# Kernel tuning notes

Measured on AMD Instinct MI355X. Metric: run time of the kernel, lower is better.

Reference implementation:

```python
import jax, jax.numpy as jnp
import numpy as np
import math

N, S, T, E, H = 2, 2048, 2048, 1024, 16
HD = E // H  # head_dim = 64


def setup_inputs() -> dict:
    key = jax.random.key(0)
    ks = jax.random.split(key, 11)
    scale = 1.0 / math.sqrt(E)
    inp = {
        "query": jax.random.normal(ks[0], (N, S, E), jnp.float32),
        "key": jax.random.normal(ks[1], (N, T, E), jnp.float32),
        "value": jax.random.normal(ks[2], (N, T, E), jnp.float32),
        "Wq": jax.random.normal(ks[3], (E, E), jnp.float32) * scale,
        "bq": jnp.zeros((E,), jnp.float32),
        "Wk": jax.random.normal(ks[4], (E, E), jnp.float32) * scale,
        "bk": jnp.zeros((E,), jnp.float32),
        "Wv": jax.random.normal(ks[5], (E, E), jnp.float32) * scale,
        "bv": jnp.zeros((E,), jnp.float32),
        "Wo": jax.random.normal(ks[6], (E, E), jnp.float32) * scale,
        "bo": jnp.zeros((E,), jnp.float32),
    }
    return inp


def reference(query, key, value, Wq, bq, Wk, bk, Wv, bv, Wo, bo):
    # QKV projections, then split heads: [N, S, E] -> [N, H, S, HD]
    q = (query @ Wq + bq).reshape(N, S, H, HD).transpose(0, 2, 1, 3)
    k = (key @ Wk + bk).reshape(N, T, H, HD).transpose(0, 2, 1, 3)
    v = (value @ Wv + bv).reshape(N, T, H, HD).transpose(0, 2, 1, 3)
    # scaled dot-product attention scores [N, H, S, T]
    scores = jnp.einsum('nhse,nhte->nhst', q, k) / math.sqrt(HD)
    attn = jax.nn.softmax(scores, axis=-1)
    # dropout is identity in eval mode
    out = jnp.einsum('nhst,nhte->nhse', attn, v)  # [N, H, S, HD]
    out = out.transpose(0, 2, 1, 3).reshape(N, S, E)
    return out @ Wo + bo
```

## Files before the change

kernel.cpp:

```cpp
#include <hip/hip_runtime.h>
#include <hip/hip_bf16.h>

typedef __bf16 bf16x8 __attribute__((ext_vector_type(8)));
typedef __bf16 bf16x4 __attribute__((ext_vector_type(4)));
typedef float  f32x4  __attribute__((ext_vector_type(4)));
typedef float  f32x16 __attribute__((ext_vector_type(16)));

#define MFMA16(a, b, c) __builtin_amdgcn_mfma_f32_16x16x32_bf16((a), (b), (c), 0, 0, 0)
#define MFMA32(a, b, c) __builtin_amdgcn_mfma_f32_32x32x16_bf16((a), (b), (c), 0, 0, 0)

constexpr int SEQ = 2048, EMB = 1024, NHEAD = 16, HD = 64;
constexpr float SSCALE = 0.18033688f;

__device__ __forceinline__ void glds16(const void* g, void* l) {
    __builtin_amdgcn_global_load_lds(
        (const __attribute__((address_space(1))) void*)g,
        (__attribute__((address_space(3))) void*)l, 16, 0, 0);
}

__global__ __launch_bounds__(256)
void prep(const float* __restrict__ W0, const float* __restrict__ W1,
          const float* __restrict__ W2, const float* __restrict__ W3,
          __bf16* __restrict__ T0, __bf16* __restrict__ T1,
          __bf16* __restrict__ T2, __bf16* __restrict__ T3,
          const float* __restrict__ X0, const float* __restrict__ X1,
          const float* __restrict__ X2, __bf16* __restrict__ Y0,
          __bf16* __restrict__ Y1, __bf16* __restrict__ Y2)
{
    __shared__ float tile[32][33];
    const int z = blockIdx.z;
    if (z < 4) {
        const float* W = (z==0) ? W0 : (z==1) ? W1 : (z==2) ? W2 : W3;
        __bf16*      T = (z==0) ? T0 : (z==1) ? T1 : (z==2) ? T2 : T3;
        const float s = (z == 0) ? SSCALE : 1.0f;
        const int kb = blockIdx.x * 32, nb = blockIdx.y * 32;
        const int c = threadIdx.x & 31, r0 = threadIdx.x >> 5;
#pragma unroll
        for (int i = 0; i < 4; ++i)
            tile[r0 + 8*i][c] = W[(size_t)(kb + r0 + 8*i)*1024 + nb + c];
        __syncthreads();
#pragma unroll
        for (int i = 0; i < 4; ++i)
            T[(size_t)(nb + r0 + 8*i)*1024 + kb + c] = (__bf16)(tile[c][r0 + 8*i] * s);
    } else {
        const float* X = (z==4) ? X0 : (z==5) ? X1 : X2;
        __bf16*      Y = (z==4) ? Y0 : (z==5) ? Y1 : Y2;
        const size_t base =
            ((size_t)(blockIdx.y * 32 + blockIdx.x) * 256 + threadIdx.x) * 16;
#pragma unroll
        for (int j = 0; j < 2; ++j) {
            const float4* s4 = (const float4*)(X + base + j*8);
            float4 f0 = s4[0], f1 = s4[1];
            bf16x8 v;
            v[0]=(__bf16)f0.x; v[1]=(__bf16)f0.y; v[2]=(__bf16)f0.z; v[3]=(__bf16)f0.w;
            v[4]=(__bf16)f1.x; v[5]=(__bf16)f1.y; v[6]=(__bf16)f1.z; v[7]=(__bf16)f1.w;
            *(bf16x8*)(Y + base + j*8) = v;
        }
    }
}

struct GArg { const __bf16* A; const __bf16* Bt; const float* bias; void* C;
              int mode; int kbase; int kcount; float bscale; };
struct GArgs3 { GArg a[3]; };

__global__ __launch_bounds__(256)
void gemmk(GArgs3 args)
{
    const GArg g = args.a[blockIdx.z];
    __shared__ __attribute__((aligned(16))) __bf16 As[128*64];
    __shared__ __attribute__((aligned(16))) __bf16 Bs[128*64];
    const int tid = threadIdx.x, lane = tid & 63, wave = tid >> 6;
    const int wm = wave >> 1, wn = wave & 1;
    const int quad = lane >> 4, l16 = lane & 15;
    const int bm = blockIdx.x, bn = blockIdx.y;

    f32x4 acc[4][4] = {};

    for (int kt = 0; kt < g.kcount; ++kt) {
        const int k0 = g.kbase + kt*64;
        __syncthreads();
#pragma unroll
        for (int j = 0; j < 4; ++j) {
            const int ci = j*256 + tid;
            const int row = ci >> 3, cg = ((ci & 7) ^ (row & 7)) * 8;
            glds16(g.A + (size_t)(bm*128 + row)*1024 + k0 + cg,
                   &As[(j*256 + wave*64)*8]);
        }
#pragma unroll
        for (int j = 0; j < 4; ++j) {
            const int ci = j*256 + tid;
            const int row = ci >> 3, cg = ((ci & 7) ^ (row & 7)) * 8;
            glds16(g.Bt + (size_t)(bn*128 + row)*1024 + k0 + cg,
                   &Bs[(j*256 + wave*64)*8]);
        }
        __syncthreads();
#pragma unroll
        for (int ks = 0; ks < 2; ++ks) {
            const int kc = ks*4 + quad;
            bf16x8 af[4], bfr[4];
#pragma unroll
            for (int mt = 0; mt < 4; ++mt) {
                const int ar = wm*64 + mt*16 + l16;
                af[mt] = *(const bf16x8*)&As[ar*64 + (kc ^ (ar & 7))*8];
            }
#pragma unroll
            for (int nt = 0; nt < 4; ++nt) {
                const int br = wn*64 + nt*16 + l16;
                bfr[nt] = *(const bf16x8*)&Bs[br*64 + (kc ^ (br & 7))*8];
            }
#pragma unroll
            for (int mt = 0; mt < 4; ++mt)
#pragma unroll
                for (int nt = 0; nt < 4; ++nt)
                    acc[mt][nt] = MFMA16(af[mt], bfr[nt], acc[mt][nt]);
        }
    }

#pragma unroll
    for (int nt = 0; nt < 4; ++nt) {
        const int n = bn*128 + wn*64 + nt*16 + l16;
        const float bvs = (g.bias ? g.bias[n] : 0.f) * g.bscale;
#pragma unroll
        for (int mt = 0; mt < 4; ++mt) {
            const int mbase = bm*128 + wm*64 + mt*16 + quad*4;
            f32x4 v = acc[mt][nt];
            if (g.mode == 0) {
                __bf16* C = (__bf16*)g.C;
                const int h = n >> 6, d = n & 63;
#pragma unroll
                for (int r = 0; r < 4; ++r) {
                    const int m = mbase + r;
                    const int nb = m >> 11, s = m & 2047;
                    C[(size_t)(nb*NHEAD + h)*(SEQ*HD) + (size_t)s*HD + d] = (__bf16)(v[r] + bvs);
                }
            } else if (g.mode == 1) {
                __bf16* C = (__bf16*)g.C;
                const int h = n >> 6, d = n & 63;
                const int nb = mbase >> 11, s = mbase & 2047;
                const int tg = (s >> 2) & 7;
                const int pg = (tg & 4) | ((tg & 1) << 1) | ((tg & 2) >> 1);
                const int sp = (s & ~31) | (pg << 2);
                bf16x4 o;
#pragma unroll
                for (int r = 0; r < 4; ++r) o[r] = (__bf16)(v[r] + bvs);
                *(bf16x4*)&C[(size_t)(nb*NHEAD + h)*(SEQ*HD) + (size_t)d*SEQ + sp] = o;
            } else {
                float* C = (float*)g.C;
#pragma unroll
                for (int r = 0; r < 4; ++r)
                    C[(size_t)(mbase + r)*1024 + n] = v[r] + bvs;
            }
        }
    }
}

__global__ __launch_bounds__(256)
void attn32(const __bf16* __restrict__ qg, const __bf16* __restrict__ kg,
            const __bf16* __restrict__ vg, __bf16* __restrict__ Og)
{
    __shared__ __attribute__((aligned(16))) __bf16 Ks[128*64];
    __shared__ __attribute__((aligned(16))) __bf16 Vs[64*128];

    const int tid = threadIdx.x, lane = tid & 63, wave = tid >> 6;
    const int l32 = lane & 31, half = lane >> 5;
    const int nh = blockIdx.y;
    const int q0 = blockIdx.x * 128;
    const __bf16* qb = qg + (size_t)nh * (SEQ*HD);
    const __bf16* kb = kg + (size_t)nh * (SEQ*HD);
    const __bf16* vb = vg + (size_t)nh * (SEQ*HD);

    bf16x8 qf[4];
#pragma unroll
    for (int ks = 0; ks < 4; ++ks)
        qf[ks] = *(const bf16x8*)(qb + (size_t)(q0 + wave*32 + l32)*HD + ks*16 + half*8);

    bf16x8 vone;
#pragma unroll
    for (int i = 0; i < 8; ++i) vone[i] = (__bf16)1.0f;

    f32x16 oacc[2] = {};
    f32x16 osum = {};

    for (int t0 = 0; t0 < SEQ; t0 += 128) {
        __syncthreads();
#pragma unroll
        for (int j = 0; j < 4; ++j) {
            const int ci = j*256 + tid;
            const int row = ci >> 3, cg = ((ci & 7) ^ (row & 7)) * 8;
            glds16(kb + (size_t)(t0 + row)*HD + cg, &Ks[(j*256 + wave*64)*8]);
        }
#pragma unroll
        for (int j = 0; j < 4; ++j) {
            const int ci = j*256 + tid;
            const int row = ci >> 4, cg = ((ci & 15) ^ (row & 7)) * 8;
            glds16(vb + (size_t)row*SEQ + t0 + cg, &Vs[(j*256 + wave*64)*8]);
        }
        __syncthreads();

        f32x16 sc[4] = {};
#pragma unroll
        for (int ks = 0; ks < 4; ++ks) {
            const int c = ks*2 + half;
#pragma unroll
            for (int nt = 0; nt < 4; ++nt) {
                const int kr = nt*32 + l32;
                bf16x8 kf = *(const bf16x8*)&Ks[kr*64 + ((c ^ (kr & 7))*8)];
                sc[nt] = MFMA32(kf, qf[ks], sc[nt]);
            }
        }

#pragma unroll
        for (int nt = 0; nt < 4; ++nt)
#pragma unroll
            for (int sub = 0; sub < 2; ++sub) {
                bf16x8 pf;
#pragma unroll
                for (int j = 0; j < 8; ++j)
                    pf[j] = (__bf16)exp2f(sc[nt][sub*8 + j]);
                const int c2 = (nt*2 + sub)*2 + half;
#pragma unroll
                for (int dt = 0; dt < 2; ++dt) {
                    const int vr = dt*32 + l32;
                    bf16x8 vf = *(const bf16x8*)&Vs[vr*128 + ((c2 ^ (vr & 7))*8)];
                    oacc[dt] = MFMA32(pf, vf, oacc[dt]);
                }
                osum = MFMA32(pf, vone, osum);
            }
    }

    const int nb = nh >> 4, h = nh & 15;
#pragma unroll
    for (int reg = 0; reg < 16; ++reg) {
        const int row = (reg & 3) + 8*(reg >> 2) + 4*half;
        const int srow = q0 + wave*32 + row;
        const float inv = 1.0f / osum[reg];
#pragma unroll
        for (int dt = 0; dt < 2; ++dt)
            Og[(size_t)(nb*SEQ + srow)*EMB + h*HD + dt*32 + l32] = (__bf16)(oacc[dt][reg] * inv);
    }
}

extern "C" void kernel_launch(void* const* d_in, const int* in_sizes, int n_in,
                              void* d_out, int out_size, void* d_ws, size_t ws_size,
                              hipStream_t stream)
{
    const float* query = (const float*)d_in[0];
    const float* key_  = (const float*)d_in[1];
    const float* value = (const float*)d_in[2];
    const float* Wq = (const float*)d_in[3];
    const float* bq = (const float*)d_in[4];
    const float* Wk = (const float*)d_in[5];
    const float* bk = (const float*)d_in[6];
    const float* Wv = (const float*)d_in[7];
    const float* bv = (const float*)d_in[8];
    const float* Wo = (const float*)d_in[9];
    const float* bo = (const float*)d_in[10];
    float* out = (float*)d_out;

    constexpr size_t SZW = 1024u*1024u;
    constexpr size_t SZX = 4096u*1024u;
    __bf16* ws  = (__bf16*)d_ws;
    __bf16* WqT = ws;
    __bf16* WkT = WqT + SZW;
    __bf16* WvT = WkT + SZW;
    __bf16* WoT = WvT + SZW;
    __bf16* xv  = WoT + SZW;
    __bf16* qh  = xv + SZX;
    __bf16* kh  = qh + SZX;
    __bf16* vTh = kh + SZX;
    __bf16* xq  = (__bf16*)d_out;
    __bf16* xk  = xq + SZX;
    __bf16* Oh  = xv;

    prep<<<dim3(32, 32, 7), 256, 0, stream>>>(Wq, Wk, Wv, Wo, WqT, WkT, WvT, WoT,
                                              query, key_, value, xq, xk, xv);
    GArgs3 a;
    a.a[0] = { xq, WqT, bq, qh,  0, 0, 16, SSCALE };
    a.a[1] = { xk, WkT, bk, kh,  0, 0, 16, 1.0f };
    a.a[2] = { xv, WvT, bv, vTh, 1, 0, 16, 1.0f };
    gemmk<<<dim3(32, 8, 3), 256, 0, stream>>>(a);
    attn32<<<dim3(16, 32), 256, 0, stream>>>(qh, kh, vTh, Oh);
    GArgs3 o;
    o.a[0] = { Oh, WoT, bo, out, 2, 0, 16, 1.0f };
    o.a[1] = o.a[0];
    o.a[2] = o.a[0];
    gemmk<<<dim3(32, 8, 1), 256, 0, stream>>>(o);
}
```

Baseline: 243.0 us.

## Split attention KV range across two wave groups and add dedicated output GEMM

The attention kernel now runs 512 threads per block, with two groups of four waves each handling half of a 256-key tile for the same 128 queries. The partial accumulators and row sums are then combined through shared memory before normalising. This doubles the waves available per query block to hide latency, at the cost of more LDS (64KB) and an extra reduction step. The output projection moves to a new smaller-tile gemmo kernel (64x128 tiles, 512 blocks) so more blocks are available to fill the GPU for the final GEMM.

Result: slower. 272.7 us (+12.2%).

```diff
diff --git a/kernel.cpp b/kernel.cpp
--- a/kernel.cpp
+++ b/kernel.cpp
@@ -133,7 +133,7 @@
                     const int nb = m >> 11, s = m & 2047;
                     C[(size_t)(nb*NHEAD + h)*(SEQ*HD) + (size_t)s*HD + d] = (__bf16)(v[r] + bvs);
                 }
-            } else if (g.mode == 1) {
+            } else {
                 __bf16* C = (__bf16*)g.C;
                 const int h = n >> 6, d = n & 63;
                 const int nb = mbase >> 11, s = mbase & 2047;
@@ -144,24 +144,87 @@
 #pragma unroll
                 for (int r = 0; r < 4; ++r) o[r] = (__bf16)(v[r] + bvs);
                 *(bf16x4*)&C[(size_t)(nb*NHEAD + h)*(SEQ*HD) + (size_t)d*SEQ + sp] = o;
-            } else {
-                float* C = (float*)g.C;
-#pragma unroll
-                for (int r = 0; r < 4; ++r)
-                    C[(size_t)(mbase + r)*1024 + n] = v[r] + bvs;
             }
         }
     }
 }
 
 __global__ __launch_bounds__(256)
+void gemmo(const __bf16* __restrict__ A, const __bf16* __restrict__ Bt,
+           const float* __restrict__ bias, float* __restrict__ C)
+{
+    __shared__ __attribute__((aligned(16))) __bf16 As[64*64];
+    __shared__ __attribute__((aligned(16))) __bf16 Bs[128*64];
+    const int tid = threadIdx.x, lane = tid & 63, wave = tid >> 6;
+    const int quad = lane >> 4, l16 = lane & 15;
+    const int bm = blockIdx.x, bn = blockIdx.y;
+
+    f32x4 acc[4][2] = {};
+
+    for (int k0 = 0; k0 < 1024; k0 += 64) {
+        __syncthreads();
+#pragma unroll
+        for (int j = 0; j < 2; ++j) {
+            const int ci = j*256 + tid;
+            const int row = ci >> 3, cg = ((ci & 7) ^ (row & 7)) * 8;
+            glds16(A + (size_t)(bm*64 + row)*1024 + k0 + cg,
+                   &As[(j*256 + wave*64)*8]);
+        }
+#pragma unroll
+        for (int j = 0; j < 4; ++j) {
+            const int ci = j*256 + tid;
+            const int row = ci >> 3, cg = ((ci & 7) ^ (row & 7)) * 8;
+            glds16(Bt + (size_t)(bn*128 + row)*1024 + k0 + cg,
+                   &Bs[(j*256 + wave*64)*8]);
+        }
+        __syncthreads();
+#pragma unroll
+        for (int ks = 0; ks < 2; ++ks) {
+            const int kc = ks*4 + quad;
+            bf16x8 af[4], bfr[2];
+#pragma unroll
+            for (int mt = 0; mt < 4; ++mt) {
+                const int ar = mt*16 + l16;
+                af[mt] = *(const bf16x8*)&As[ar*64 + (kc ^ (ar & 7))*8];
+            }
+#pragma unroll
+            for (int nt = 0; nt < 2; ++nt) {
+                const int br = wave*32 + nt*16 + l16;
+                bfr[nt] = *(const bf16x8*)&Bs[br*64 + (kc ^ (br & 7))*8];
+            }
+#pragma unroll
+            for (int mt = 0; mt < 4; ++mt)
+#pragma unroll
+                for (int nt = 0; nt < 2; ++nt)
+                    acc[mt][nt] = MFMA16(af[mt], bfr[nt], acc[mt][nt]);
+        }
+    }
+#pragma unroll
+    for (int nt = 0; nt < 2; ++nt) {
+        const int n = bn*128 + wave*32 + nt*16 + l16;
+        const float bv = bias[n];
+#pragma unroll
+        for (int mt = 0; mt < 4; ++mt) {
+            const int mbase = bm*64 + mt*16 + quad*4;
+            f32x4 v = acc[mt][nt];
+#pragma unroll
+            for (int r = 0; r < 4; ++r)
+                C[(size_t)(mbase + r)*1024 + n] = v[r] + bv;
+        }
+    }
+}
+
+__global__ __launch_bounds__(512, 4)
 void attn32(const __bf16* __restrict__ qg, const __bf16* __restrict__ kg,
             const __bf16* __restrict__ vg, __bf16* __restrict__ Og)
 {
-    __shared__ __attribute__((aligned(16))) __bf16 Ks[128*64];
-    __shared__ __attribute__((aligned(16))) __bf16 Vs[64*128];
+    __shared__ __attribute__((aligned(16))) char smem[64*1024];
+    __bf16* Ks = (__bf16*)smem;
+    __bf16* Vs = (__bf16*)(smem + 32768);
+    float*  Xch = (float*)smem;
 
     const int tid = threadIdx.x, lane = tid & 63, wave = tid >> 6;
+    const int w4 = wave & 3, grp = wave >> 2;
     const int l32 = lane & 31, half = lane >> 5;
     const int nh = blockIdx.y;
     const int q0 = blockIdx.x * 128;
@@ -172,7 +235,7 @@
     bf16x8 qf[4];
 #pragma unroll
     for (int ks = 0; ks < 4; ++ks)
-        qf[ks] = *(const bf16x8*)(qb + (size_t)(q0 + wave*32 + l32)*HD + ks*16 + half*8);
+        qf[ks] = *(const bf16x8*)(qb + (size_t)(q0 + w4*32 + l32)*HD + ks*16 + half*8);
 
     bf16x8 vone;
 #pragma unroll
@@ -181,19 +244,20 @@
     f32x16 oacc[2] = {};
     f32x16 osum = {};
 
-    for (int t0 = 0; t0 < SEQ; t0 += 128) {
-        __syncthreads();
-#pragma unroll
-        for (int j = 0; j < 4; ++j) {
-            const int ci = j*256 + tid;
-            const int row = ci >> 3, cg = ((ci & 7) ^ (row & 7)) * 8;
-            glds16(kb + (size_t)(t0 + row)*HD + cg, &Ks[(j*256 + wave*64)*8]);
-        }
-#pragma unroll
-        for (int j = 0; j < 4; ++j) {
-            const int ci = j*256 + tid;
-            const int row = ci >> 4, cg = ((ci & 15) ^ (row & 7)) * 8;
-            glds16(vb + (size_t)row*SEQ + t0 + cg, &Vs[(j*256 + wave*64)*8]);
+    for (int t0 = 0; t0 < SEQ; t0 += 256) {
+        __syncthreads();
+#pragma unroll
+        for (int j = 0; j < 4; ++j) {
+            const int ci = j*512 + tid;
+            const int row = ci >> 3, cg = ((ci & 7) ^ (row & 7)) * 8;
+            glds16(kb + (size_t)(t0 + row)*HD + cg, &Ks[(j*512 + wave*64)*8]);
+        }
+#pragma unroll
+        for (int j = 0; j < 4; ++j) {
+            const int ci = j*512 + tid;
+            const int row = ci >> 5, pos = ci & 31;
+            const int cg = ((pos & ~7) | ((pos & 7) ^ (row & 7))) * 8;
+            glds16(vb + (size_t)row*SEQ + t0 + cg, &Vs[(j*512 + wave*64)*8]);
         }
         __syncthreads();
 
@@ -203,7 +267,7 @@
             const int c = ks*2 + half;
 #pragma unroll
             for (int nt = 0; nt < 4; ++nt) {
-                const int kr = nt*32 + l32;
+                const int kr = grp*128 + nt*32 + l32;
                 bf16x8 kf = *(const bf16x8*)&Ks[kr*64 + ((c ^ (kr & 7))*8)];
                 sc[nt] = MFMA32(kf, qf[ks], sc[nt]);
             }
@@ -217,26 +281,48 @@
 #pragma unroll
                 for (int j = 0; j < 8; ++j)
                     pf[j] = (__bf16)exp2f(sc[nt][sub*8 + j]);
-                const int c2 = (nt*2 + sub)*2 + half;
+                const int c2 = grp*16 + (nt*2 + sub)*2 + half;
 #pragma unroll
                 for (int dt = 0; dt < 2; ++dt) {
                     const int vr = dt*32 + l32;
-                    bf16x8 vf = *(const bf16x8*)&Vs[vr*128 + ((c2 ^ (vr & 7))*8)];
+                    const int pos = (c2 & ~7) | ((c2 & 7) ^ (vr & 7));
+                    bf16x8 vf = *(const bf16x8*)&Vs[vr*256 + pos*8];
                     oacc[dt] = MFMA32(pf, vf, oacc[dt]);
                 }
                 osum = MFMA32(pf, vone, osum);
             }
     }
 
-    const int nb = nh >> 4, h = nh & 15;
-#pragma unroll
-    for (int reg = 0; reg < 16; ++reg) {
-        const int row = (reg & 3) + 8*(reg >> 2) + 4*half;
-        const int srow = q0 + wave*32 + row;
-        const float inv = 1.0f / osum[reg];
-#pragma unroll
-        for (int dt = 0; dt < 2; ++dt)
-            Og[(size_t)(nb*SEQ + srow)*EMB + h*HD + dt*32 + l32] = (__bf16)(oacc[dt][reg] * inv);
+    __syncthreads();
+    if (grp == 1) {
+        float* dst = &Xch[((w4*64) + lane) * 48];
+#pragma unroll
+        for (int i = 0; i < 16; ++i) {
+            dst[i]      = oacc[0][i];
+            dst[16 + i] = oacc[1][i];
+            dst[32 + i] = osum[i];
+        }
+    }
+    __syncthreads();
+    if (grp == 0) {
+        const float* src = &Xch[((w4*64) + lane) * 48];
+#pragma unroll
+        for (int i = 0; i < 16; ++i) {
+            oacc[0][i] += src[i];
+            oacc[1][i] += src[16 + i];
+            osum[i]    += src[32 + i];
+        }
+        const int nb = nh >> 4, h = nh & 15;
+#pragma unroll
+        for (int reg = 0; reg < 16; ++reg) {
+            const int row = (reg & 3) + 8*(reg >> 2) + 4*half;
+            const int srow = q0 + w4*32 + row;
+            const float inv = 1.0f / osum[reg];
+#pragma unroll
+            for (int dt = 0; dt < 2; ++dt)
+                Og[(size_t)(nb*SEQ + srow)*EMB + h*HD + dt*32 + l32] =
+                    (__bf16)(oacc[dt][reg] * inv);
+        }
     }
 }
 
@@ -279,10 +365,6 @@
     a.a[1] = { xk, WkT, bk, kh,  0, 0, 16, 1.0f };
     a.a[2] = { xv, WvT, bv, vTh, 1, 0, 16, 1.0f };
     gemmk<<<dim3(32, 8, 3), 256, 0, stream>>>(a);
-    attn32<<<dim3(16, 32), 256, 0, stream>>>(qh, kh, vTh, Oh);
-    GArgs3 o;
-    o.a[0] = { Oh, WoT, bo, out, 2, 0, 16, 1.0f };
-    o.a[1] = o.a[0];
-    o.a[2] = o.a[0];
-    gemmk<<<dim3(32, 8, 1), 256, 0, stream>>>(o);
-}
+    attn32<<<dim3(16, 32), 512, 0, stream>>>(qh, kh, vTh, Oh);
+    gemmo<<<dim3(64, 8), 256, 0, stream>>>(Oh, WoT, bo, out);
+}
```
